# Optimization experiments

Hardware: AMD Instinct MI355X
Metric: run time of the kernel (lower is better)

Reference implementation:

```python
import jax, jax.numpy as jnp
import numpy as np

N = 50000       # nodes
E = 800000      # edges (avg degree 16)
IN_F = 128
OUT_F = 128
NEG_SLOPE = 0.2  # LeakyReLU alpha
EPS = 1e-10


def setup_inputs() -> dict:
    key = jax.random.key(0)
    k1, k2, k3, k4 = jax.random.split(key, 4)
    h = jax.random.normal(k1, (N, IN_F), dtype=jnp.float32)
    edge_index = jax.random.randint(k2, (2, E), 0, N, dtype=jnp.int32)
    # nn.Linear(in, out, bias=False): weight is [out, in], Wh = h @ W.T
    W = jax.random.normal(k3, (OUT_F, IN_F), dtype=jnp.float32) * (1.0 / np.sqrt(IN_F))
    # a: [2*out, 1], xavier_uniform with gain=1.414
    lim = 1.414 * np.sqrt(6.0 / (2 * OUT_F + 1))
    a = jax.random.uniform(k4, (2 * OUT_F, 1), dtype=jnp.float32, minval=-lim, maxval=lim)
    return {"h": h, "edge_index": edge_index, "W": W, "a": a}


def reference(h, edge_index, W, a):
    Wh = h @ W.T                              # [N, out]
    rows = edge_index[0]
    cols = edge_index[1]
    # cat([Wh_i, Wh_j],1) @ a  ==  (Wh @ a1)[rows] + (Wh @ a2)[cols]
    a1 = a[:OUT_F, 0]
    a2 = a[OUT_F:, 0]
    s1 = Wh @ a1                              # [N]
    s2 = Wh @ a2                              # [N]
    e = jax.nn.leaky_relu(s1[rows] + s2[cols], negative_slope=NEG_SLOPE)  # [E]
    e = e - jnp.max(e)
    exp_e = jnp.exp(e)
    sum_exp = jax.ops.segment_sum(exp_e, rows, num_segments=N)            # [N]
    alpha = exp_e / (sum_exp[rows] + EPS)                                 # [E]
    # sparse.mm(adj_att, Wh): h_prime[i] = sum_j alpha_ij * Wh[j]
    h_prime = jax.ops.segment_sum(alpha[:, None] * Wh[cols], rows, num_segments=N)
    return jax.nn.elu(h_prime)
```

## Files before the change

kernel.cpp:

```cpp
#include <hip/hip_runtime.h>

constexpr int FD = 128;
constexpr int NBMAX = 512;
constexpr int CH1 = 2048;
constexpr int CAPB = 3072;

typedef __attribute__((ext_vector_type(8))) short short8;
typedef __attribute__((ext_vector_type(4))) float floatx4;

__device__ __forceinline__ unsigned fenc(float f) {
    unsigned u = __float_as_uint(f);
    return (u & 0x80000000u) ? ~u : (u | 0x80000000u);
}
__device__ __forceinline__ float fdec(unsigned e) {
    return (e & 0x80000000u) ? __uint_as_float(e & 0x7fffffffu)
                             : __uint_as_float(~e);
}

__device__ __forceinline__ unsigned bpack(float x, float y) {
    unsigned ux = __float_as_uint(x); ux += 0x7FFFu + ((ux >> 16) & 1u);
    unsigned uy = __float_as_uint(y); uy += 0x7FFFu + ((uy >> 16) & 1u);
    return (ux >> 16) | (uy & 0xFFFF0000u);
}

__global__ __launch_bounds__(128) void initwt_kernel(const float* __restrict__ W,
                                                     unsigned* __restrict__ Wb,
                                                     int* __restrict__ bcursor,
                                                     unsigned* __restrict__ maxslot) {
    int j = blockIdx.x, k = threadIdx.x;
    float w = W[(size_t)j * FD + k];
    float pw = __shfl_xor(w, 1, 64);
    if ((k & 1) == 0) Wb[(size_t)j * 64 + (k >> 1)] = bpack(w, pw);
    if (j == 0) {
        for (int i = k; i < NBMAX; i += 128) bcursor[i] = 0;
        if (k < 2) maxslot[k] = 0x007FFFFFu;
    }
}

union GBShared {
    struct {
        int cnt[NBMAX];
        int ex[NBMAX];
        int gbase[NBMAX];
        int wtot[8];
        unsigned stage[CH1];
    } bin;
    struct {
        float m1[8];
        float m2[8];
    } gm;
};

__global__ __launch_bounds__(512) void gembin_kernel(const float* __restrict__ h,
                                                     const unsigned* __restrict__ Wb,
                                                     const float* __restrict__ a,
                                                     const int* __restrict__ ei,
                                                     int* __restrict__ bcursor,
                                                     unsigned* __restrict__ Whb,
                                                     float* __restrict__ s1,
                                                     float* __restrict__ s2,
                                                     unsigned* __restrict__ ebuf,
                                                     unsigned* __restrict__ maxslot,
                                                     int n, int e_cnt, int ngemm) {
    __shared__ GBShared sh;
    int t = threadIdx.x;

    if ((int)blockIdx.x < ngemm) {
        int w = t >> 6, lane = t & 63;
        int quad = lane >> 4, c = lane & 15;
        int rbase = blockIdx.x * 128 + w * 16;
        int node = rbase + c;

        int arow = min(node, n - 1);
        const float4* hrow = (const float4*)(h + (size_t)arow * FD);
        union { uint4 u; short8 s; } hf[4];
#pragma unroll
        for (int kk = 0; kk < 4; ++kk) {
            int k0 = kk * 32 + quad * 8;
            float4 f0 = hrow[k0 >> 2];
            float4 f1 = hrow[(k0 >> 2) + 1];
            hf[kk].u.x = bpack(f0.x, f0.y);
            hf[kk].u.y = bpack(f0.z, f0.w);
            hf[kk].u.z = bpack(f1.x, f1.y);
            hf[kk].u.w = bpack(f1.z, f1.w);
        }

        float p1 = 0.f, p2 = 0.f;

#pragma unroll
        for (int tt = 0; tt < 8; ++tt) {
            const uint4* wrow = (const uint4*)(Wb + (size_t)(tt * 16 + c) * 64 + quad * 4);
            floatx4 acc = {0.f, 0.f, 0.f, 0.f};
#pragma unroll
            for (int kk = 0; kk < 4; ++kk) {
                union { uint4 u; short8 s; } wf;
                wf.u = wrow[kk * 4];
                acc = __builtin_amdgcn_mfma_f32_16x16x32_bf16(wf.s, hf[kk].s, acc, 0, 0, 0);
            }
            float4 a1q = *(const float4*)(a + tt * 16 + quad * 4);
            float4 a2q = *(const float4*)(a + FD + tt * 16 + quad * 4);
            p1 = fmaf(acc[0], a1q.x, p1); p1 = fmaf(acc[1], a1q.y, p1);
            p1 = fmaf(acc[2], a1q.z, p1); p1 = fmaf(acc[3], a1q.w, p1);
            p2 = fmaf(acc[0], a2q.x, p2); p2 = fmaf(acc[1], a2q.y, p2);
            p2 = fmaf(acc[2], a2q.z, p2); p2 = fmaf(acc[3], a2q.w, p2);
            if (node < n) {
                uint2 pk2;
                pk2.x = bpack(acc[0], acc[1]);
                pk2.y = bpack(acc[2], acc[3]);
                *(uint2*)(Whb + (size_t)node * 64 + tt * 8 + quad * 2) = pk2;
            }
        }

        p1 += __shfl_xor(p1, 16, 64); p1 += __shfl_xor(p1, 32, 64);
        p2 += __shfl_xor(p2, 16, 64); p2 += __shfl_xor(p2, 32, 64);
        if (quad == 0 && node < n) { s1[node] = p1; s2[node] = p2; }

        float m1 = (node < n) ? p1 : -3.0e38f;
        float m2 = (node < n) ? p2 : -3.0e38f;
#pragma unroll
        for (int d = 1; d < 16; d <<= 1) {
            m1 = fmaxf(m1, __shfl_xor(m1, d, 64));
            m2 = fmaxf(m2, __shfl_xor(m2, d, 64));
        }
        if (lane == 0) { sh.gm.m1[w] = m1; sh.gm.m2[w] = m2; }
        __syncthreads();
        if (t == 0) {
            float g1 = -3.0e38f, g2 = -3.0e38f;
#pragma unroll
            for (int k = 0; k < 8; ++k) {
                g1 = fmaxf(g1, sh.gm.m1[k]);
                g2 = fmaxf(g2, sh.gm.m2[k]);
            }
            atomicMax(&maxslot[0], fenc(g1));
            atomicMax(&maxslot[1], fenc(g2));
        }
    } else {
        int bb = blockIdx.x - ngemm;
        sh.bin.cnt[t] = 0;
        __syncthreads();
        int base = bb * CH1;
        int m = min(CH1, e_cnt - base);

        unsigned pack[4];
        int rank[4], bkt[4];
        int nk = 0;
#pragma unroll
        for (int k = 0; k < 4; ++k) {
            int idx = t + k * 512;
            if (idx < m) {
                int ed = base + idx;
                int r = ei[ed];
                int cc = ei[e_cnt + ed];
                unsigned p = ((unsigned)r << 16) | (unsigned)cc;
                int b = r >> 7;
                pack[nk] = p;
                bkt[nk] = b;
                rank[nk] = atomicAdd(&sh.bin.cnt[b], 1);
                ++nk;
            }
        }
        __syncthreads();

        int l = t & 63, w = t >> 6;
        int v = sh.bin.cnt[t];
        int iv = v;
#pragma unroll
        for (int d = 1; d < 64; d <<= 1) {
            int u = __shfl_up(iv, d, 64);
            if (l >= d) iv += u;
        }
        if (l == 63) sh.bin.wtot[w] = iv;
        __syncthreads();
        if (t == 0) {
            int s = 0;
#pragma unroll
            for (int k = 0; k < 8; ++k) { int x = sh.bin.wtot[k]; sh.bin.wtot[k] = s; s += x; }
        }
        __syncthreads();
        int excl = iv - v + sh.bin.wtot[w];
        sh.bin.ex[t] = excl;
        if (v > 0) sh.bin.gbase[t] = atomicAdd(&bcursor[t], v);
        __syncthreads();
        for (int k = 0; k < nk; ++k)
            sh.bin.stage[sh.bin.ex[bkt[k]] + rank[k]] = pack[k];
        __syncthreads();
        for (int s = t; s < m; s += 512) {
            unsigned p = sh.bin.stage[s];
            int b = p >> 23;
            int pos = sh.bin.gbase[b] + (s - sh.bin.ex[b]);
            if (pos < CAPB) ebuf[(size_t)b * CAPB + pos] = p;
        }
    }
}

#define FMA8(bv, av)                                                    \
    acc[0] = fmaf(av, __uint_as_float((bv).x << 16), acc[0]);           \
    acc[1] = fmaf(av, __uint_as_float((bv).x & 0xFFFF0000u), acc[1]);   \
    acc[2] = fmaf(av, __uint_as_float((bv).y << 16), acc[2]);           \
    acc[3] = fmaf(av, __uint_as_float((bv).y & 0xFFFF0000u), acc[3]);   \
    acc[4] = fmaf(av, __uint_as_float((bv).z << 16), acc[4]);           \
    acc[5] = fmaf(av, __uint_as_float((bv).z & 0xFFFF0000u), acc[5]);   \
    acc[6] = fmaf(av, __uint_as_float((bv).w << 16), acc[6]);           \
    acc[7] = fmaf(av, __uint_as_float((bv).w & 0xFFFF0000u), acc[7]);

__global__ __launch_bounds__(1024) void agg_kernel(const unsigned* __restrict__ ebuf,
                                                   const int* __restrict__ bcnt,
                                                   const float* __restrict__ s1,
                                                   const float* __restrict__ s2,
                                                   const unsigned* __restrict__ Whb,
                                                   const unsigned* __restrict__ maxslot,
                                                   float* __restrict__ out, int n) {
    __shared__ uint2 pairs[CAPB];
    __shared__ int cnt[128];
    __shared__ int exs[128];
    __shared__ float invs[128];
    __shared__ float s1l[128];
    int b = blockIdx.x;
    int t = threadIdx.x;
    int row0 = b << 7;
    int m = min(bcnt[b], CAPB);

    if (t < 128) {
        cnt[t] = 0;
        int gr = row0 + t;
        s1l[t] = (gr < n) ? s1[gr] : 0.f;
    }
    __syncthreads();

    unsigned pk[3];
    int rk[3], lrr[3];
    float s2v[3];
    int nk = 0;
#pragma unroll
    for (int k = 0; k < 3; ++k) {
        int idx = t + (k << 10);
        if (idx < m) {
            unsigned p = ebuf[(size_t)b * CAPB + idx];
            int lr = (p >> 16) & 127;
            pk[nk] = p;
            lrr[nk] = lr;
            s2v[nk] = s2[p & 0xFFFFu];
            rk[nk] = atomicAdd(&cnt[lr], 1);
            ++nk;
        }
    }
    __syncthreads();

    if (t < 64) {
        int va = cnt[t], vb = cnt[t + 64];
        int ia = va, ib = vb;
#pragma unroll
        for (int d = 1; d < 64; d <<= 1) {
            int ua = __shfl_up(ia, d, 64);
            int ub = __shfl_up(ib, d, 64);
            if (t >= d) { ia += ua; ib += ub; }
        }
        int tot = __shfl(ia, 63, 64);
        exs[t] = ia - va;
        exs[t + 64] = tot + ib - vb;
    }
    __syncthreads();

    float M = fdec(maxslot[0]) + fdec(maxslot[1]);
    M = (M >= 0.f) ? M : 0.2f * M;

    for (int k = 0; k < nk; ++k) {
        unsigned p = pk[k];
        float sv = s1l[lrr[k]] + s2v[k];
        float le = (sv >= 0.f) ? sv : 0.2f * sv;
        float ev = __expf(le - M);
        pairs[exs[lrr[k]] + rk[k]] = make_uint2(p & 0xFFFFu, __float_as_uint(ev));
    }
    __syncthreads();

    {
        int hw = t >> 5, fl = t & 31;
        for (int r = hw; r < 128; r += 32) {
            int s0 = exs[r], d = cnt[r];
            float s = 0.f;
            for (int k2 = fl; k2 < d; k2 += 32)
                s += __uint_as_float(pairs[s0 + k2].y);
#pragma unroll
            for (int dd = 1; dd < 32; dd <<= 1)
                s += __shfl_xor(s, dd, 64);
            if (fl == 0) invs[r] = 1.0f / (s + 1e-10f);
        }
    }
    __syncthreads();

    int w = t >> 6, l = t & 63, q = l >> 4, fl2 = l & 15;
    for (int ni = (w << 3); ni < (w << 3) + 8; ++ni) {
        int node = row0 + ni;
        if (node >= n) break;
        int s0 = exs[ni], deg = cnt[ni];
        float acc[8] = {0.f, 0.f, 0.f, 0.f, 0.f, 0.f, 0.f, 0.f};
        int j = q;
        for (; j + 4 < deg; j += 8) {
            uint2 e0 = pairs[s0 + j];
            uint2 e1 = pairs[s0 + j + 4];
            uint4 b0 = *(const uint4*)(Whb + (size_t)e0.x * 64 + 4 * fl2);
            uint4 b1 = *(const uint4*)(Whb + (size_t)e1.x * 64 + 4 * fl2);
            float a0 = __uint_as_float(e0.y);
            float a1 = __uint_as_float(e1.y);
            FMA8(b0, a0)
            FMA8(b1, a1)
        }
        if (j < deg) {
            uint2 e0 = pairs[s0 + j];
            uint4 b0 = *(const uint4*)(Whb + (size_t)e0.x * 64 + 4 * fl2);
            float a0 = __uint_as_float(e0.y);
            FMA8(b0, a0)
        }
#pragma unroll
        for (int i = 0; i < 8; ++i) {
            acc[i] += __shfl_xor(acc[i], 16, 64);
            acc[i] += __shfl_xor(acc[i], 32, 64);
        }
        if (q < 2) {
            float inv = invs[ni];
            float v0 = (q ? acc[4] : acc[0]) * inv;
            float v1 = (q ? acc[5] : acc[1]) * inv;
            float v2 = (q ? acc[6] : acc[2]) * inv;
            float v3 = (q ? acc[7] : acc[3]) * inv;
            float4 r;
            r.x = (v0 > 0.f) ? v0 : expm1f(v0);
            r.y = (v1 > 0.f) ? v1 : expm1f(v1);
            r.z = (v2 > 0.f) ? v2 : expm1f(v2);
            r.w = (v3 > 0.f) ? v3 : expm1f(v3);
            *((float4*)(out + (size_t)node * FD + fl2 * 8 + q * 4)) = r;
        }
    }
}

extern "C" void kernel_launch(void* const* d_in, const int* in_sizes, int n_in,
                              void* d_out, int out_size, void* d_ws, size_t ws_size,
                              hipStream_t stream) {
    const float* h = (const float*)d_in[0];
    const int* ei  = (const int*)d_in[1];
    const float* W = (const float*)d_in[2];
    const float* a = (const float*)d_in[3];
    float* out = (float*)d_out;
    int n = in_sizes[0] / FD;
    int e = in_sizes[1] / 2;
    int nb = (n + 127) >> 7;

    char* ws = (char*)d_ws;
    size_t off = 0;
    auto alloc = [&](size_t bytes) -> void* {
        void* p = ws + off;
        off += bytes;
        off = (off + 255) & ~(size_t)255;
        return p;
    };
    unsigned* Whb     = (unsigned*)alloc((size_t)n * 64 * sizeof(unsigned));
    unsigned* Wb      = (unsigned*)alloc((size_t)FD * 64 * sizeof(unsigned));
    float*    s1      = (float*)alloc((size_t)n * sizeof(float));
    float*    s2      = (float*)alloc((size_t)n * sizeof(float));
    int*      bcursor = (int*)alloc((size_t)NBMAX * sizeof(int));
    unsigned* ebuf    = (unsigned*)alloc((size_t)NBMAX * CAPB * sizeof(unsigned));
    unsigned* maxslot = (unsigned*)alloc(2 * sizeof(unsigned));

    int ngemm = (n + 127) / 128;
    int nbin = (e + CH1 - 1) / CH1;

    initwt_kernel<<<FD, 128, 0, stream>>>(W, Wb, bcursor, maxslot);
    gembin_kernel<<<ngemm + nbin, 512, 0, stream>>>(h, Wb, a, ei, bcursor, Whb,
                                                    s1, s2, ebuf, maxslot, n, e, ngemm);
    agg_kernel<<<nb, 1024, 0, stream>>>(ebuf, bcursor, s1, s2, Whb, maxslot, out, n);
}
```

Baseline: 145.1 us.

## Shrink aggregation buckets to 32 rows and bin edges with direct global atomics

Buckets shrink from 128 to 32 rows. The aggregation kernel now runs many more 256-thread blocks, and the GEMM kernel handles 64 rows per block. Shared-memory staged binning is replaced by a per-edge global atomicAdd on the bucket cursor. The separate softmax-sum pass becomes shared-memory atomic accumulation. The change also adds nontemporal loads and stores and unrolls the gather loop four ways. The aim is better load balance and occupancy and less synchronisation, at the cost of heavier contention on global atomics and loss of coalesced bucket writes.

```diff
diff --git a/kernel.cpp b/kernel.cpp
--- a/kernel.cpp
+++ b/kernel.cpp
@@ -1,9 +1,10 @@
 #include <hip/hip_runtime.h>
 
 constexpr int FD = 128;
-constexpr int NBMAX = 512;
-constexpr int CH1 = 2048;
-constexpr int CAPB = 3072;
+constexpr int BSH = 5;
+constexpr int BROWS = 32;
+constexpr int NBMAX = 2048;
+constexpr int CAPB = 768;
 
 typedef __attribute__((ext_vector_type(8))) short short8;
 typedef __attribute__((ext_vector_type(4))) float floatx4;
@@ -37,21 +38,7 @@
     }
 }
 
-union GBShared {
-    struct {
-        int cnt[NBMAX];
-        int ex[NBMAX];
-        int gbase[NBMAX];
-        int wtot[8];
-        unsigned stage[CH1];
-    } bin;
-    struct {
-        float m1[8];
-        float m2[8];
-    } gm;
-};
-
-__global__ __launch_bounds__(512) void gembin_kernel(const float* __restrict__ h,
+__global__ __launch_bounds__(256) void gembin_kernel(const float* __restrict__ h,
                                                      const unsigned* __restrict__ Wb,
                                                      const float* __restrict__ a,
                                                      const int* __restrict__ ei,
@@ -61,24 +48,24 @@
                                                      float* __restrict__ s2,
                                                      unsigned* __restrict__ ebuf,
                                                      unsigned* __restrict__ maxslot,
-                                                     int n, int e_cnt, int ngemm) {
-    __shared__ GBShared sh;
+                                                     int n, int e_cnt, int ngemm, int nbin) {
     int t = threadIdx.x;
 
     if ((int)blockIdx.x < ngemm) {
+        __shared__ float m1s[4], m2s[4];
         int w = t >> 6, lane = t & 63;
         int quad = lane >> 4, c = lane & 15;
-        int rbase = blockIdx.x * 128 + w * 16;
+        int rbase = blockIdx.x * 64 + w * 16;
         int node = rbase + c;
 
         int arow = min(node, n - 1);
-        const float4* hrow = (const float4*)(h + (size_t)arow * FD);
+        const floatx4* hrow = (const floatx4*)(h + (size_t)arow * FD);
         union { uint4 u; short8 s; } hf[4];
 #pragma unroll
         for (int kk = 0; kk < 4; ++kk) {
             int k0 = kk * 32 + quad * 8;
-            float4 f0 = hrow[k0 >> 2];
-            float4 f1 = hrow[(k0 >> 2) + 1];
+            floatx4 f0 = __builtin_nontemporal_load(hrow + (k0 >> 2));
+            floatx4 f1 = __builtin_nontemporal_load(hrow + (k0 >> 2) + 1);
             hf[kk].u.x = bpack(f0.x, f0.y);
             hf[kk].u.y = bpack(f0.z, f0.w);
             hf[kk].u.z = bpack(f1.x, f1.y);
@@ -122,73 +109,27 @@
             m1 = fmaxf(m1, __shfl_xor(m1, d, 64));
             m2 = fmaxf(m2, __shfl_xor(m2, d, 64));
         }
-        if (lane == 0) { sh.gm.m1[w] = m1; sh.gm.m2[w] = m2; }
+        if (lane == 0) { m1s[w] = m1; m2s[w] = m2; }
         __syncthreads();
         if (t == 0) {
             float g1 = -3.0e38f, g2 = -3.0e38f;
 #pragma unroll
-            for (int k = 0; k < 8; ++k) {
-                g1 = fmaxf(g1, sh.gm.m1[k]);
-                g2 = fmaxf(g2, sh.gm.m2[k]);
+            for (int k = 0; k < 4; ++k) {
+                g1 = fmaxf(g1, m1s[k]);
+                g2 = fmaxf(g2, m2s[k]);
             }
             atomicMax(&maxslot[0], fenc(g1));
             atomicMax(&maxslot[1], fenc(g2));
         }
     } else {
-        int bb = blockIdx.x - ngemm;
-        sh.bin.cnt[t] = 0;
-        __syncthreads();
-        int base = bb * CH1;
-        int m = min(CH1, e_cnt - base);
-
-        unsigned pack[4];
-        int rank[4], bkt[4];
-        int nk = 0;
-#pragma unroll
-        for (int k = 0; k < 4; ++k) {
-            int idx = t + k * 512;
-            if (idx < m) {
-                int ed = base + idx;
-                int r = ei[ed];
-                int cc = ei[e_cnt + ed];
-                unsigned p = ((unsigned)r << 16) | (unsigned)cc;
-                int b = r >> 7;
-                pack[nk] = p;
-                bkt[nk] = b;
-                rank[nk] = atomicAdd(&sh.bin.cnt[b], 1);
-                ++nk;
-            }
-        }
-        __syncthreads();
-
-        int l = t & 63, w = t >> 6;
-        int v = sh.bin.cnt[t];
-        int iv = v;
-#pragma unroll
-        for (int d = 1; d < 64; d <<= 1) {
-            int u = __shfl_up(iv, d, 64);
-            if (l >= d) iv += u;
-        }
-        if (l == 63) sh.bin.wtot[w] = iv;
-        __syncthreads();
-        if (t == 0) {
-            int s = 0;
-#pragma unroll
-            for (int k = 0; k < 8; ++k) { int x = sh.bin.wtot[k]; sh.bin.wtot[k] = s; s += x; }
-        }
-        __syncthreads();
-        int excl = iv - v + sh.bin.wtot[w];
-        sh.bin.ex[t] = excl;
-        if (v > 0) sh.bin.gbase[t] = atomicAdd(&bcursor[t], v);
-        __syncthreads();
-        for (int k = 0; k < nk; ++k)
-            sh.bin.stage[sh.bin.ex[bkt[k]] + rank[k]] = pack[k];
-        __syncthreads();
-        for (int s = t; s < m; s += 512) {
-            unsigned p = sh.bin.stage[s];
-            int b = p >> 23;
-            int pos = sh.bin.gbase[b] + (s - sh.bin.ex[b]);
-            if (pos < CAPB) ebuf[(size_t)b * CAPB + pos] = p;
+        int stride = nbin * 256;
+        for (int i = ((int)blockIdx.x - ngemm) * 256 + t; i < e_cnt; i += stride) {
+            int r  = __builtin_nontemporal_load(ei + i);
+            int cc = __builtin_nontemporal_load(ei + e_cnt + i);
+            unsigned p = ((unsigned)r << 16) | (unsigned)cc;
+            int bk = r >> BSH;
+            int pos = atomicAdd(&bcursor[bk], 1);
+            if (pos < CAPB) ebuf[(size_t)bk * CAPB + pos] = p;
         }
     }
 }
@@ -203,25 +144,27 @@
     acc[6] = fmaf(av, __uint_as_float((bv).w << 16), acc[6]);           \
     acc[7] = fmaf(av, __uint_as_float((bv).w & 0xFFFF0000u), acc[7]);
 
-__global__ __launch_bounds__(1024) void agg_kernel(const unsigned* __restrict__ ebuf,
-                                                   const int* __restrict__ bcnt,
-                                                   const float* __restrict__ s1,
-                                                   const float* __restrict__ s2,
-                                                   const unsigned* __restrict__ Whb,
-                                                   const unsigned* __restrict__ maxslot,
-                                                   float* __restrict__ out, int n) {
+__global__ __launch_bounds__(256) void agg_kernel(const unsigned* __restrict__ ebuf,
+                                                  const int* __restrict__ bcnt,
+                                                  const float* __restrict__ s1,
+                                                  const float* __restrict__ s2,
+                                                  const unsigned* __restrict__ Whb,
+                                                  const unsigned* __restrict__ maxslot,
+                                                  float* __restrict__ out, int n) {
     __shared__ uint2 pairs[CAPB];
-    __shared__ int cnt[128];
-    __shared__ int exs[128];
-    __shared__ float invs[128];
-    __shared__ float s1l[128];
+    __shared__ int cnt[BROWS];
+    __shared__ int exs[BROWS];
+    __shared__ float sums[BROWS];
+    __shared__ float invs[BROWS];
+    __shared__ float s1l[BROWS];
     int b = blockIdx.x;
     int t = threadIdx.x;
-    int row0 = b << 7;
+    int row0 = b << BSH;
     int m = min(bcnt[b], CAPB);
 
-    if (t < 128) {
+    if (t < BROWS) {
         cnt[t] = 0;
+        sums[t] = 0.f;
         int gr = row0 + t;
         s1l[t] = (gr < n) ? s1[gr] : 0.f;
     }
@@ -233,10 +176,10 @@
     int nk = 0;
 #pragma unroll
     for (int k = 0; k < 3; ++k) {
-        int idx = t + (k << 10);
+        int idx = t + (k << 8);
         if (idx < m) {
-            unsigned p = ebuf[(size_t)b * CAPB + idx];
-            int lr = (p >> 16) & 127;
+            unsigned p = __builtin_nontemporal_load(ebuf + (size_t)b * CAPB + idx);
+            int lr = (p >> 16) & (BROWS - 1);
             pk[nk] = p;
             lrr[nk] = lr;
             s2v[nk] = s2[p & 0xFFFFu];
@@ -246,18 +189,15 @@
     }
     __syncthreads();
 
-    if (t < 64) {
-        int va = cnt[t], vb = cnt[t + 64];
-        int ia = va, ib = vb;
-#pragma unroll
-        for (int d = 1; d < 64; d <<= 1) {
-            int ua = __shfl_up(ia, d, 64);
-            int ub = __shfl_up(ib, d, 64);
-            if (t >= d) { ia += ua; ib += ub; }
-        }
-        int tot = __shfl(ia, 63, 64);
-        exs[t] = ia - va;
-        exs[t + 64] = tot + ib - vb;
+    if (t < BROWS) {
+        int v = cnt[t];
+        int iv = v;
+#pragma unroll
+        for (int d = 1; d < BROWS; d <<= 1) {
+            int u = __shfl_up(iv, d, 64);
+            if (t >= d) iv += u;
+        }
+        exs[t] = iv - v;
     }
     __syncthreads();
 
@@ -270,22 +210,10 @@
         float le = (sv >= 0.f) ? sv : 0.2f * sv;
         float ev = __expf(le - M);
         pairs[exs[lrr[k]] + rk[k]] = make_uint2(p & 0xFFFFu, __float_as_uint(ev));
-    }
-    __syncthreads();
-
-    {
-        int hw = t >> 5, fl = t & 31;
-        for (int r = hw; r < 128; r += 32) {
-            int s0 = exs[r], d = cnt[r];
-            float s = 0.f;
-            for (int k2 = fl; k2 < d; k2 += 32)
-                s += __uint_as_float(pairs[s0 + k2].y);
-#pragma unroll
-            for (int dd = 1; dd < 32; dd <<= 1)
-                s += __shfl_xor(s, dd, 64);
-            if (fl == 0) invs[r] = 1.0f / (s + 1e-10f);
-        }
-    }
+        atomicAdd(&sums[lrr[k]], ev);
+    }
+    __syncthreads();
+    if (t < BROWS) invs[t] = 1.0f / (sums[t] + 1e-10f);
     __syncthreads();
 
     int w = t >> 6, l = t & 63, q = l >> 4, fl2 = l & 15;
@@ -295,17 +223,25 @@
         int s0 = exs[ni], deg = cnt[ni];
         float acc[8] = {0.f, 0.f, 0.f, 0.f, 0.f, 0.f, 0.f, 0.f};
         int j = q;
-        for (; j + 4 < deg; j += 8) {
+        for (; j + 12 < deg; j += 16) {
             uint2 e0 = pairs[s0 + j];
             uint2 e1 = pairs[s0 + j + 4];
+            uint2 e2 = pairs[s0 + j + 8];
+            uint2 e3 = pairs[s0 + j + 12];
             uint4 b0 = *(const uint4*)(Whb + (size_t)e0.x * 64 + 4 * fl2);
             uint4 b1 = *(const uint4*)(Whb + (size_t)e1.x * 64 + 4 * fl2);
+            uint4 b2 = *(const uint4*)(Whb + (size_t)e2.x * 64 + 4 * fl2);
+            uint4 b3 = *(const uint4*)(Whb + (size_t)e3.x * 64 + 4 * fl2);
             float a0 = __uint_as_float(e0.y);
             float a1 = __uint_as_float(e1.y);
+            float a2 = __uint_as_float(e2.y);
+            float a3 = __uint_as_float(e3.y);
             FMA8(b0, a0)
             FMA8(b1, a1)
-        }
-        if (j < deg) {
+            FMA8(b2, a2)
+            FMA8(b3, a3)
+        }
+        for (; j < deg; j += 4) {
             uint2 e0 = pairs[s0 + j];
             uint4 b0 = *(const uint4*)(Whb + (size_t)e0.x * 64 + 4 * fl2);
             float a0 = __uint_as_float(e0.y);
@@ -322,12 +258,12 @@
             float v1 = (q ? acc[5] : acc[1]) * inv;
             float v2 = (q ? acc[6] : acc[2]) * inv;
             float v3 = (q ? acc[7] : acc[3]) * inv;
-            float4 r;
+            floatx4 r;
             r.x = (v0 > 0.f) ? v0 : expm1f(v0);
             r.y = (v1 > 0.f) ? v1 : expm1f(v1);
             r.z = (v2 > 0.f) ? v2 : expm1f(v2);
             r.w = (v3 > 0.f) ? v3 : expm1f(v3);
-            *((float4*)(out + (size_t)node * FD + fl2 * 8 + q * 4)) = r;
+            __builtin_nontemporal_store(r, (floatx4*)(out + (size_t)node * FD + fl2 * 8 + q * 4));
         }
     }
 }
@@ -342,7 +278,7 @@
     float* out = (float*)d_out;
     int n = in_sizes[0] / FD;
     int e = in_sizes[1] / 2;
-    int nb = (n + 127) >> 7;
+    int nb = (n + BROWS - 1) >> BSH;
 
     char* ws = (char*)d_ws;
     size_t off = 0;
@@ -360,11 +296,11 @@
     unsigned* ebuf    = (unsigned*)alloc((size_t)NBMAX * CAPB * sizeof(unsigned));
     unsigned* maxslot = (unsigned*)alloc(2 * sizeof(unsigned));
 
-    int ngemm = (n + 127) / 128;
-    int nbin = (e + CH1 - 1) / CH1;
+    int ngemm = (n + 63) / 64;
+    int nbin  = ngemm;
 
     initwt_kernel<<<FD, 128, 0, stream>>>(W, Wb, bcursor, maxslot);
-    gembin_kernel<<<ngemm + nbin, 512, 0, stream>>>(h, Wb, a, ei, bcursor, Whb,
-                                                    s1, s2, ebuf, maxslot, n, e, ngemm);
-    agg_kernel<<<nb, 1024, 0, stream>>>(ebuf, bcursor, s1, s2, Whb, maxslot, out, n);
-}
+    gembin_kernel<<<ngemm + nbin, 256, 0, stream>>>(h, Wb, a, ei, bcursor, Whb,
+                                                    s1, s2, ebuf, maxslot, n, e, ngemm, nbin);
+    agg_kernel<<<nb, 256, 0, stream>>>(ebuf, bcursor, s1, s2, Whb, maxslot, out, n);
+}
```

Result: slower. 242.3 us (+67.0%).
